# Performance work log

Hardware: AMD Instinct MI355X
Metric: run time of the kernel (lower is better)

Reference implementation:

```python
import jax, jax.numpy as jnp
import numpy as np

D_MODEL = 4096
NUM_HEADS = 4
D_HEAD = D_MODEL // (2 * NUM_HEADS)  # 512, must equal seq_len for lambda broadcast
LAMBDA_INIT = 0.8


def setup_inputs() -> dict:
    key = jax.random.key(0)
    ks = jax.random.split(key, 12)
    B, S = 8, 512
    s_in = 1.0 / np.sqrt(D_MODEL)
    return {
        "x": jax.random.normal(ks[0], (B, S, D_MODEL), jnp.float32),
        "wq_w": jax.random.normal(ks[1], (2 * D_MODEL, D_MODEL), jnp.float32) * s_in,
        "wq_b": jnp.zeros((2 * D_MODEL,), jnp.float32),
        "wk_w": jax.random.normal(ks[2], (2 * D_MODEL, D_MODEL), jnp.float32) * s_in,
        "wk_b": jnp.zeros((2 * D_MODEL,), jnp.float32),
        "wv_w": jax.random.normal(ks[3], (2 * D_MODEL, D_MODEL), jnp.float32) * s_in,
        "wv_b": jnp.zeros((2 * D_MODEL,), jnp.float32),
        "lambda_q1": jax.random.uniform(ks[4], (D_HEAD,), jnp.float32),
        "lambda_k1": jax.random.uniform(ks[5], (D_HEAD,), jnp.float32),
        "lambda_q2": jax.random.uniform(ks[6], (D_HEAD,), jnp.float32),
        "lambda_k2": jax.random.uniform(ks[7], (D_HEAD,), jnp.float32),
    }


def reference(x, wq_w, wq_b, wk_w, wk_b, wv_w, wv_b,
              lambda_q1, lambda_k1, lambda_q2, lambda_k2):
    # Projections: d_model -> 2*d_model, then chunk q/k into two halves
    q = x @ wq_w.T + wq_b                      # [B,S,2D]
    k = x @ wk_w.T + wk_b                      # [B,S,2D]
    v = x @ wv_w.T + wv_b                      # [B,S,2D]
    q1, q2 = jnp.split(q, 2, axis=-1)          # each [B,S,D]
    k1, k2 = jnp.split(k, 2, axis=-1)

    # lambda_value: [d_head], broadcast over last (key) axis of scores
    lam = jnp.exp(lambda_q1 * lambda_k1) - jnp.exp(lambda_q2 * lambda_k2) + LAMBDA_INIT

    scale = 1.0 / jnp.sqrt(jnp.float32(D_HEAD))
    a1 = jax.nn.softmax(jnp.einsum("bqd,bkd->bqk", q1, k1) * scale, axis=-1)
    a2 = jax.nn.softmax(jnp.einsum("bqd,bkd->bqk", q2, k2) * scale, axis=-1)
    scores = a1 - lam * a2                     # lam: [S]==[d_head] broadcast on key dim
    return jnp.einsum("bqk,bkd->bqd", scores, v)
```

## Files before the change

kernel.cpp:

```cpp
#include <hip/hip_runtime.h>
#include <hip/hip_bf16.h>
#include <stdint.h>

#define DM 4096
#define TWO_DM 8192
#define BATCH 8
#define SEQ 512
#define BS_ROWS (BATCH*SEQ)
#define LAMBDA_INIT 0.8f

typedef float f32x4 __attribute__((ext_vector_type(4)));
typedef __bf16 bf16x8 __attribute__((ext_vector_type(8)));

static __device__ __forceinline__ unsigned short f2bf(float f) {
  __hip_bfloat16 h = __float2bfloat16(f);
  return __builtin_bit_cast(unsigned short, h);
}

__global__ __launch_bounds__(256) void cast_f32_to_bf16(
    const float* __restrict__ in, unsigned short* __restrict__ out, int n4) {
  int stride = gridDim.x * 256;
  for (int i = blockIdx.x * 256 + threadIdx.x; i < n4; i += stride) {
    f32x4 v = reinterpret_cast<const f32x4*>(in)[i];
    ushort4 o;
    o.x = f2bf(v[0]); o.y = f2bf(v[1]); o.z = f2bf(v[2]); o.w = f2bf(v[3]);
    reinterpret_cast<ushort4*>(out)[i] = o;
  }
}

template<int MODE, int HAS_BIAS>
__global__ __launch_bounds__(256) void gemm_bt(
    const unsigned short* __restrict__ A, const unsigned short* __restrict__ B,
    void* __restrict__ C, const float* __restrict__ bias,
    int K, int lda, int ldb, int ldc,
    long aSB, long aSH, long bSB, long bSH, long cSZ, float scale)
{
  __shared__ unsigned short lA[128 * 32];
  __shared__ unsigned short lB[128 * 32];

  const int tid  = threadIdx.x;
  const int lane = tid & 63;
  const int wave = tid >> 6;
  const int wr = wave >> 1, wc = wave & 1;
  const int row0 = blockIdx.y * 128;
  const int col0 = blockIdx.x * 128;
  const int z  = blockIdx.z;
  const int zb = z & 7, zh = z >> 3;

  const unsigned short* Ap = A + (long)zb * aSB + (long)zh * aSH;
  const unsigned short* Bp = B + (long)zb * bSB + (long)zh * bSH;

  f32x4 acc[4][4] = {};

  const int f0 = tid,        r0 = f0 >> 2, c0 = (f0 & 3) * 8;
  const int f1 = tid + 256,  r1 = f1 >> 2, c1 = (f1 & 3) * 8;

  for (int k0 = 0; k0 < K; k0 += 32) {
    __builtin_amdgcn_global_load_lds(
        (const __attribute__((address_space(1))) void*)(Ap + (long)(row0 + r0) * lda + k0 + c0),
        (__attribute__((address_space(3))) void*)(lA + f0 * 8), 16, 0, 0);
    __builtin_amdgcn_global_load_lds(
        (const __attribute__((address_space(1))) void*)(Ap + (long)(row0 + r1) * lda + k0 + c1),
        (__attribute__((address_space(3))) void*)(lA + f1 * 8), 16, 0, 0);
    __builtin_amdgcn_global_load_lds(
        (const __attribute__((address_space(1))) void*)(Bp + (long)(col0 + r0) * ldb + k0 + c0),
        (__attribute__((address_space(3))) void*)(lB + f0 * 8), 16, 0, 0);
    __builtin_amdgcn_global_load_lds(
        (const __attribute__((address_space(1))) void*)(Bp + (long)(col0 + r1) * ldb + k0 + c1),
        (__attribute__((address_space(3))) void*)(lB + f1 * 8), 16, 0, 0);
    __syncthreads();

    bf16x8 af[4], bfr[4];
    #pragma unroll
    for (int m = 0; m < 4; ++m)
      af[m] = *reinterpret_cast<const bf16x8*>(
          &lA[(wr * 64 + m * 16 + (lane & 15)) * 32 + (lane >> 4) * 8]);
    #pragma unroll
    for (int n = 0; n < 4; ++n)
      bfr[n] = *reinterpret_cast<const bf16x8*>(
          &lB[(wc * 64 + n * 16 + (lane & 15)) * 32 + (lane >> 4) * 8]);
    #pragma unroll
    for (int m = 0; m < 4; ++m)
      #pragma unroll
      for (int n = 0; n < 4; ++n)
        acc[m][n] = __builtin_amdgcn_mfma_f32_16x16x32_bf16(af[m], bfr[n], acc[m][n], 0, 0, 0);
    __syncthreads();
  }

  const long cOff = (long)z * cSZ;
  const int rbase = row0 + wr * 64;
  const int cbase = col0 + wc * 64;
  #pragma unroll
  for (int m = 0; m < 4; ++m) {
    #pragma unroll
    for (int n = 0; n < 4; ++n) {
      const int c = cbase + n * 16 + (lane & 15);
      const float bv = HAS_BIAS ? bias[c] : 0.0f;
      if (MODE == 2) {
        const int r  = rbase + m * 16 + (lane >> 4) * 4;
        const int b  = r >> 9, s0 = r & 511;
        ushort4 o;
        o.x = f2bf(acc[m][n][0] * scale + bv);
        o.y = f2bf(acc[m][n][1] * scale + bv);
        o.z = f2bf(acc[m][n][2] * scale + bv);
        o.w = f2bf(acc[m][n][3] * scale + bv);
        *reinterpret_cast<ushort4*>(
            (unsigned short*)C + ((long)b * TWO_DM + c) * SEQ + s0) = o;
      } else {
        #pragma unroll
        for (int j = 0; j < 4; ++j) {
          const int r = rbase + m * 16 + (lane >> 4) * 4 + j;
          const float v = acc[m][n][j] * scale + bv;
          if (MODE == 1) ((unsigned short*)C)[cOff + (long)r * ldc + c] = f2bf(v);
          else           ((float*)C)[cOff + (long)r * ldc + c] = v;
        }
      }
    }
  }
}

__global__ __launch_bounds__(512) void softmax_combine(
    const float* __restrict__ S,
    const float* __restrict__ lq1, const float* __restrict__ lk1,
    const float* __restrict__ lq2, const float* __restrict__ lk2,
    unsigned short* __restrict__ P)
{
  __shared__ float red[16];
  const int row = blockIdx.x;
  const int k = threadIdx.x;
  const int lane = k & 63, wid = k >> 6;
  const long off = (long)row * SEQ;
  float v1 = S[off + k];
  float v2 = S[(long)8 * SEQ * SEQ + off + k];
  float m1 = v1, m2 = v2;
  #pragma unroll
  for (int o = 32; o; o >>= 1) { m1 = fmaxf(m1, __shfl_xor(m1, o)); m2 = fmaxf(m2, __shfl_xor(m2, o)); }
  if (lane == 0) { red[wid] = m1; red[8 + wid] = m2; }
  __syncthreads();
  m1 = red[0]; m2 = red[8];
  #pragma unroll
  for (int i = 1; i < 8; ++i) { m1 = fmaxf(m1, red[i]); m2 = fmaxf(m2, red[8 + i]); }
  __syncthreads();
  const float e1 = __expf(v1 - m1), e2 = __expf(v2 - m2);
  float s1 = e1, s2 = e2;
  #pragma unroll
  for (int o = 32; o; o >>= 1) { s1 += __shfl_xor(s1, o); s2 += __shfl_xor(s2, o); }
  if (lane == 0) { red[wid] = s1; red[8 + wid] = s2; }
  __syncthreads();
  s1 = 0.f; s2 = 0.f;
  #pragma unroll
  for (int i = 0; i < 8; ++i) { s1 += red[i]; s2 += red[8 + i]; }
  const float lam = __expf(lq1[k] * lk1[k]) - __expf(lq2[k] * lk2[k]) + LAMBDA_INIT;
  P[off + k] = f2bf(e1 / s1 - lam * (e2 / s2));
}

extern "C" void kernel_launch(void* const* d_in, const int* in_sizes, int n_in,
                              void* d_out, int out_size, void* d_ws, size_t ws_size,
                              hipStream_t stream) {
  const float* x    = (const float*)d_in[0];
  const float* wq_w = (const float*)d_in[1];
  const float* wq_b = (const float*)d_in[2];
  const float* wk_w = (const float*)d_in[3];
  const float* wk_b = (const float*)d_in[4];
  const float* wv_w = (const float*)d_in[5];
  const float* wv_b = (const float*)d_in[6];
  const float* lq1  = (const float*)d_in[7];
  const float* lk1  = (const float*)d_in[8];
  const float* lq2  = (const float*)d_in[9];
  const float* lk2  = (const float*)d_in[10];

  const size_t MB = 1024ull * 1024;

  if (ws_size < 160 * MB) {
    hipMemsetAsync(d_out, 0, (size_t)out_size * sizeof(float), stream);
    return;
  }

  char* ws = (char*)d_ws;
  unsigned short* xb   = (unsigned short*)(ws);
  float*          sbuf = (float*)(ws);
  unsigned short* pb   = (unsigned short*)(ws + 16 * MB);
  unsigned short* vtb  = (unsigned short*)(ws + 32 * MB);
  unsigned short* wb   = (unsigned short*)(ws + 96 * MB);
  unsigned short* qb   = (unsigned short*)(d_out);
  unsigned short* kb   = (unsigned short*)((char*)d_out + 64 * MB);

  const float scaleQK = 0.04419417382415922f;

  cast_f32_to_bf16<<<2048, 256, 0, stream>>>(x, xb, (BS_ROWS * DM) / 4);

  cast_f32_to_bf16<<<2048, 256, 0, stream>>>(wv_w, wb, (TWO_DM * DM) / 4);
  gemm_bt<2, 1><<<dim3(TWO_DM / 128, BS_ROWS / 128, 1), 256, 0, stream>>>(
      xb, wb, vtb, wv_b, DM, DM, DM, 0, 0, 0, 0, 0, 0, 1.0f);
  cast_f32_to_bf16<<<2048, 256, 0, stream>>>(wq_w, wb, (TWO_DM * DM) / 4);
  gemm_bt<1, 1><<<dim3(TWO_DM / 128, BS_ROWS / 128, 1), 256, 0, stream>>>(
      xb, wb, qb, wq_b, DM, DM, DM, TWO_DM, 0, 0, 0, 0, 0, 1.0f);
  cast_f32_to_bf16<<<2048, 256, 0, stream>>>(wk_w, wb, (TWO_DM * DM) / 4);
  gemm_bt<1, 1><<<dim3(TWO_DM / 128, BS_ROWS / 128, 1), 256, 0, stream>>>(
      xb, wb, kb, wk_b, DM, DM, DM, TWO_DM, 0, 0, 0, 0, 0, 1.0f);

  gemm_bt<0, 0><<<dim3(SEQ / 128, SEQ / 128, 16), 256, 0, stream>>>(
      qb, kb, sbuf, nullptr, DM, TWO_DM, TWO_DM, SEQ,
      (long)SEQ * TWO_DM, DM, (long)SEQ * TWO_DM, DM, (long)SEQ * SEQ, scaleQK);

  softmax_combine<<<BS_ROWS, 512, 0, stream>>>(sbuf, lq1, lk1, lq2, lk2, pb);

  gemm_bt<0, 0><<<dim3(TWO_DM / 128, SEQ / 128, 8), 256, 0, stream>>>(
      pb, vtb, (float*)d_out, nullptr, SEQ, SEQ, SEQ, TWO_DM,
      (long)SEQ * SEQ, 0, (long)TWO_DM * SEQ, 0, (long)SEQ * TWO_DM, 1.0f);
}
```

Measured before the change: 1.704 ms.

## Add 256x256 double-buffered pipelined GEMM for QKV projections

Replaces the 128x128 single-stage projection GEMM with a 256x256-tile, 512-thread kernel. It double-buffers 64-wide K slices in LDS, XOR-swizzles the LDS layout to avoid bank conflicts, interleaves global_load_lds staging with MFMA phases using explicit barriers, waitcnt and setprio, and swizzles the block order for L2 locality. The goal is to hide global-load latency and raise data reuse in the three dominant projection GEMMs. The cost is 128KB of LDS per block and a heavily hand-scheduled kernel that only works when K is a multiple of 128.

```diff
diff --git a/kernel.cpp b/kernel.cpp
--- a/kernel.cpp
+++ b/kernel.cpp
@@ -25,6 +25,140 @@
     ushort4 o;
     o.x = f2bf(v[0]); o.y = f2bf(v[1]); o.z = f2bf(v[2]); o.w = f2bf(v[3]);
     reinterpret_cast<ushort4*>(out)[i] = o;
+  }
+}
+
+#define STG(SMAT, SBUF, SKS, SKT)                                              \
+  {                                                                            \
+    const unsigned short* _s0 = ((SMAT) ? b_src0 : a_src0) + (SKT)*64 + (SKS)*32; \
+    const unsigned short* _s1 = ((SMAT) ? b_src1 : a_src1) + (SKT)*64 + (SKS)*32; \
+    unsigned short* _d = lds + ((SMAT)?32768:0) + ((SBUF)*2+(SKS))*8192 + tid*8;  \
+    __builtin_amdgcn_global_load_lds((const __attribute__((address_space(1))) void*)_s0, \
+        (__attribute__((address_space(3))) void*)_d, 16, 0, 0);                \
+    __builtin_amdgcn_global_load_lds((const __attribute__((address_space(1))) void*)_s1, \
+        (__attribute__((address_space(3))) void*)(_d + 4096), 16, 0, 0);       \
+  }
+
+#define PHASE(BUF, KS, MO, RB, DOSTG, SMAT, SBUF, SKS, SKT, DOVM)              \
+  {                                                                            \
+    _Pragma("unroll") for (int m = 0; m < 4; ++m) {                            \
+      const int row = wm*128 + ((MO)+m)*16 + fr;                               \
+      const int gp = g ^ (row & 3) ^ ((row >> 2) & 3);                         \
+      af[m] = *reinterpret_cast<const bf16x8*>(                                \
+          lds + ((BUF)*2+(KS))*8192 + row*32 + gp*8);                          \
+    }                                                                          \
+    if (RB) {                                                                  \
+      _Pragma("unroll") for (int n = 0; n < 4; ++n) {                          \
+        const int row = wn*64 + n*16 + fr;                                     \
+        const int gp = g ^ (row & 3) ^ ((row >> 2) & 3);                       \
+        bfr[n] = *reinterpret_cast<const bf16x8*>(                             \
+            lds + 32768 + ((BUF)*2+(KS))*8192 + row*32 + gp*8);                \
+      }                                                                        \
+    }                                                                          \
+    if (DOSTG) STG(SMAT, SBUF, SKS, SKT);                                      \
+    __builtin_amdgcn_sched_barrier(0);                                         \
+    __builtin_amdgcn_s_barrier();                                              \
+    __builtin_amdgcn_s_setprio(1);                                             \
+    _Pragma("unroll") for (int m = 0; m < 4; ++m)                              \
+      _Pragma("unroll") for (int n = 0; n < 4; ++n)                            \
+        acc[(MO)+m][n] = __builtin_amdgcn_mfma_f32_16x16x32_bf16(              \
+            af[m], bfr[n], acc[(MO)+m][n], 0, 0, 0);                           \
+    __builtin_amdgcn_s_setprio(0);                                             \
+    __builtin_amdgcn_sched_barrier(0);                                         \
+    if (DOVM) { asm volatile("s_waitcnt vmcnt(6)" ::: "memory"); }             \
+    __builtin_amdgcn_s_barrier();                                              \
+  }
+
+template<int MODE>
+__global__ __launch_bounds__(512, 2) void gemm256_proj(
+    const unsigned short* __restrict__ A, const unsigned short* __restrict__ B,
+    void* __restrict__ C, const float* __restrict__ bias,
+    int K, int lda, int ldb, int ldc)
+{
+  __shared__ unsigned short lds[65536];
+
+  const int tid  = threadIdx.x;
+  const int lane = tid & 63;
+  const int wid  = tid >> 6;
+  const int wm = wid >> 2;
+  const int wn = wid & 3;
+  const int fr = lane & 15;
+  const int g  = lane >> 4;
+
+  const int nwg  = gridDim.x * gridDim.y;
+  const int flat = blockIdx.y * gridDim.x + blockIdx.x;
+  const int swz  = (flat & 7) * (nwg >> 3) + (flat >> 3);
+  const int bx = swz % gridDim.x;
+  const int by = swz / gridDim.x;
+  const int row0 = by * 256;
+  const int col0 = bx * 256;
+
+  const int srow = tid >> 2;
+  const int gq   = (tid & 3) ^ ((tid >> 2) & 3) ^ ((tid >> 4) & 3);
+  const unsigned short* a_src0 = A + (long)(row0 + srow) * lda + gq * 8;
+  const unsigned short* a_src1 = A + (long)(row0 + 128 + srow) * lda + gq * 8;
+  const unsigned short* b_src0 = B + (long)(col0 + srow) * ldb + gq * 8;
+  const unsigned short* b_src1 = B + (long)(col0 + 128 + srow) * ldb + gq * 8;
+
+  f32x4 acc[8][4] = {};
+  bf16x8 af[4], bfr[4];
+
+  STG(1,0,0, 0); STG(0,0,0, 0); STG(1,0,1, 0); STG(0,0,1, 0);
+  asm volatile("s_waitcnt vmcnt(4)" ::: "memory");
+  STG(1,1,0, 1); STG(0,1,0, 1); STG(1,1,1, 1);
+  asm volatile("s_waitcnt vmcnt(6)" ::: "memory");
+  __builtin_amdgcn_s_barrier();
+
+  const int nt = K >> 6;
+  for (int i = 0; i <= nt/2 - 2; ++i) {
+    const int t = 2 * i;
+    PHASE(0,0,0, 1, 1, 0,1,1, t+1, 0)
+    PHASE(0,0,4, 0, 1, 1,0,0, t+2, 0)
+    PHASE(0,1,0, 1, 1, 0,0,0, t+2, 0)
+    PHASE(0,1,4, 0, 1, 1,0,1, t+2, 1)
+    PHASE(1,0,0, 1, 1, 0,0,1, t+2, 0)
+    PHASE(1,0,4, 0, 1, 1,1,0, t+3, 0)
+    PHASE(1,1,0, 1, 1, 0,1,0, t+3, 0)
+    PHASE(1,1,4, 0, 1, 1,1,1, t+3, 1)
+  }
+  STG(0,1,1, nt-1);
+  asm volatile("s_waitcnt vmcnt(0)" ::: "memory");
+  __builtin_amdgcn_s_barrier();
+  PHASE(0,0,0, 1, 0, 0,0,0,0, 0)
+  PHASE(0,0,4, 0, 0, 0,0,0,0, 0)
+  PHASE(0,1,0, 1, 0, 0,0,0,0, 0)
+  PHASE(0,1,4, 0, 0, 0,0,0,0, 0)
+  PHASE(1,0,0, 1, 0, 0,0,0,0, 0)
+  PHASE(1,0,4, 0, 0, 0,0,0,0, 0)
+  PHASE(1,1,0, 1, 0, 0,0,0,0, 0)
+  PHASE(1,1,4, 0, 0, 0,0,0,0, 0)
+
+  const int rb0 = row0 + wm * 128;
+  const int cb0 = col0 + wn * 64;
+  #pragma unroll
+  for (int m = 0; m < 8; ++m) {
+    #pragma unroll
+    for (int n = 0; n < 4; ++n) {
+      const int c = cb0 + n * 16 + fr;
+      const float bv = bias[c];
+      if (MODE == 2) {
+        const int r  = rb0 + m * 16 + g * 4;
+        const int b  = r >> 9, s0 = r & 511;
+        ushort4 o;
+        o.x = f2bf(acc[m][n][0] + bv);
+        o.y = f2bf(acc[m][n][1] + bv);
+        o.z = f2bf(acc[m][n][2] + bv);
+        o.w = f2bf(acc[m][n][3] + bv);
+        *reinterpret_cast<ushort4*>(
+            (unsigned short*)C + ((long)b * TWO_DM + c) * SEQ + s0) = o;
+      } else {
+        #pragma unroll
+        for (int j = 0; j < 4; ++j) {
+          const int r = rb0 + m * 16 + g * 4 + j;
+          ((unsigned short*)C)[(long)r * ldc + c] = f2bf(acc[m][n][j] + bv);
+        }
+      }
+    }
   }
 }
 
@@ -96,24 +230,12 @@
     for (int n = 0; n < 4; ++n) {
       const int c = cbase + n * 16 + (lane & 15);
       const float bv = HAS_BIAS ? bias[c] : 0.0f;
-      if (MODE == 2) {
-        const int r  = rbase + m * 16 + (lane >> 4) * 4;
-        const int b  = r >> 9, s0 = r & 511;
-        ushort4 o;
-        o.x = f2bf(acc[m][n][0] * scale + bv);
-        o.y = f2bf(acc[m][n][1] * scale + bv);
-        o.z = f2bf(acc[m][n][2] * scale + bv);
-        o.w = f2bf(acc[m][n][3] * scale + bv);
-        *reinterpret_cast<ushort4*>(
-            (unsigned short*)C + ((long)b * TWO_DM + c) * SEQ + s0) = o;
-      } else {
-        #pragma unroll
-        for (int j = 0; j < 4; ++j) {
-          const int r = rbase + m * 16 + (lane >> 4) * 4 + j;
-          const float v = acc[m][n][j] * scale + bv;
-          if (MODE == 1) ((unsigned short*)C)[cOff + (long)r * ldc + c] = f2bf(v);
-          else           ((float*)C)[cOff + (long)r * ldc + c] = v;
-        }
+      #pragma unroll
+      for (int j = 0; j < 4; ++j) {
+        const int r = rbase + m * 16 + (lane >> 4) * 4 + j;
+        const float v = acc[m][n][j] * scale + bv;
+        if (MODE == 1) ((unsigned short*)C)[cOff + (long)r * ldc + c] = f2bf(v);
+        else           ((float*)C)[cOff + (long)r * ldc + c] = v;
       }
     }
   }
@@ -170,7 +292,6 @@
   const float* lk2  = (const float*)d_in[10];
 
   const size_t MB = 1024ull * 1024;
-
   if (ws_size < 160 * MB) {
     hipMemsetAsync(d_out, 0, (size_t)out_size * sizeof(float), stream);
     return;
@@ -186,18 +307,16 @@
   unsigned short* kb   = (unsigned short*)((char*)d_out + 64 * MB);
 
   const float scaleQK = 0.04419417382415922f;
+  const dim3 pgrid(TWO_DM / 256, BS_ROWS / 256, 1);
 
   cast_f32_to_bf16<<<2048, 256, 0, stream>>>(x, xb, (BS_ROWS * DM) / 4);
 
   cast_f32_to_bf16<<<2048, 256, 0, stream>>>(wv_w, wb, (TWO_DM * DM) / 4);
-  gemm_bt<2, 1><<<dim3(TWO_DM / 128, BS_ROWS / 128, 1), 256, 0, stream>>>(
-      xb, wb, vtb, wv_b, DM, DM, DM, 0, 0, 0, 0, 0, 0, 1.0f);
+  gemm256_proj<2><<<pgrid, 512, 0, stream>>>(xb, wb, vtb, wv_b, DM, DM, DM, 0);
   cast_f32_to_bf16<<<2048, 256, 0, stream>>>(wq_w, wb, (TWO_DM * DM) / 4);
-  gemm_bt<1, 1><<<dim3(TWO_DM / 128, BS_ROWS / 128, 1), 256, 0, stream>>>(
-      xb, wb, qb, wq_b, DM, DM, DM, TWO_DM, 0, 0, 0, 0, 0, 1.0f);
+  gemm256_proj<1><<<pgrid, 512, 0, stream>>>(xb, wb, qb, wq_b, DM, DM, DM, TWO_DM);
   cast_f32_to_bf16<<<2048, 256, 0, stream>>>(wk_w, wb, (TWO_DM * DM) / 4);
-  gemm_bt<1, 1><<<dim3(TWO_DM / 128, BS_ROWS / 128, 1), 256, 0, stream>>>(
-      xb, wb, kb, wk_b, DM, DM, DM, TWO_DM, 0, 0, 0, 0, 0, 1.0f);
+  gemm256_proj<1><<<pgrid, 512, 0, stream>>>(xb, wb, kb, wk_b, DM, DM, DM, TWO_DM);
 
   gemm_bt<0, 0><<<dim3(SEQ / 128, SEQ / 128, 16), 256, 0, stream>>>(
       qb, kb, sbuf, nullptr, DM, TWO_DM, TWO_DM, SEQ,
```

After: 1.417 ms. 16.9% less time.
